# Kernel tuning notes

Measured on AMD Instinct MI355X. Metric: run time of the kernel, lower is better.

## Reference

```python
import jax, jax.numpy as jnp
import numpy as np
from jax import lax

H = 145; W = 145; BANDS = 200; D_MODEL = 128; NUM_CLASSES = 17
# Mamba2 defaults: expand=2, headdim=64, d_state=128, d_conv=4, ngroups=1
D_INNER = 256; NHEADS = 4; HEADDIM = 64; D_STATE = 128; D_CONV = 4
D_IN_PROJ = 2 * D_INNER + 2 * D_STATE + NHEADS  # 772
CONV_DIM = D_INNER + 2 * D_STATE                # 512


def _gelu(x):
    return jax.nn.gelu(x, approximate=False)


def _ln(x, g, b, eps=1e-5):
    m = jnp.mean(x, -1, keepdims=True)
    v = jnp.mean((x - m) ** 2, -1, keepdims=True)
    return (x - m) * lax.rsqrt(v + eps) * g + b


def _adaptive_pool_last(x, out):
    # PyTorch AdaptiveAvgPool semantics along the last axis via integral image
    L = x.shape[-1]
    i = np.arange(out)
    starts = (i * L) // out
    ends = -((-(i + 1) * L) // out)  # ceil((i+1)*L/out)
    cs = jnp.concatenate([jnp.zeros(x.shape[:-1] + (1,), x.dtype), jnp.cumsum(x, -1)], -1)
    return (cs[..., ends] - cs[..., starts]) / jnp.asarray(ends - starts, x.dtype)


def _mamba2(u, in_w, conv_w, conv_b, dt_bias, A_log, D, norm_w, out_w):
    # u: (L, D_MODEL). Faithful Mamba2 reference path (batch=1 squeezed).
    L = u.shape[0]
    zxbcdt = u @ in_w                      # (L, 772)
    z = zxbcdt[:, :D_INNER]                # (L, 256)
    xBC = zxbcdt[:, D_INNER:2 * D_INNER + 2 * D_STATE]  # (L, 512)
    dt = jax.nn.softplus(zxbcdt[:, -NHEADS:] + dt_bias)  # (L, 4)
    # causal depthwise conv1d, kernel D_CONV, then SiLU
    xp = jnp.pad(xBC, ((D_CONV - 1, 0), (0, 0)))
    xBC = sum(xp[k:k + L] * conv_w[:, k] for k in range(D_CONV)) + conv_b
    xBC = jax.nn.silu(xBC)
    xh = xBC[:, :D_INNER].reshape(L, NHEADS, HEADDIM)     # (L, h, p)
    Bm = xBC[:, D_INNER:D_INNER + D_STATE]                # (L, n)
    Cm = xBC[:, D_INNER + D_STATE:]                       # (L, n)
    A = -jnp.exp(A_log)                                   # (h,)

    def step(state, inp):
        dt_t, x_t, B_t, C_t = inp          # (h,), (h,p), (n,), (n,)
        dA = jnp.exp(dt_t * A)             # (h,)
        state = state * dA[:, None, None] + (dt_t[:, None] * x_t)[:, :, None] * B_t[None, None, :]
        y_t = jnp.einsum('hpn,n->hp', state, C_t)
        return state, y_t

    s0 = jnp.zeros((NHEADS, HEADDIM, D_STATE), u.dtype)
    _, y = lax.scan(step, s0, (dt, xh, Bm, Cm))           # y: (L, h, p)
    y = y + D[None, :, None] * xh
    y = y.reshape(L, D_INNER) * jax.nn.silu(z)            # gated
    y = y * lax.rsqrt(jnp.mean(y * y, -1, keepdims=True) + 1e-5) * norm_w  # RMSNormGated
    return y @ out_w                                      # (L, D_MODEL)


def _forward(x, ln_pre_g, ln_pre_b, fe_w1, fe_b1, fe_w2, fe_b2,
             cv_w1, cv_b1, cv_w2, cv_b2, mp_w, mp_b, mp_ln_g, mp_ln_b,
             m_in_w, m_conv_w, m_conv_b, m_dt_bias, m_A_log, m_D, m_norm_w, m_out_w,
             cls_ln_g, cls_ln_b, cls_w1, cls_b1, cls_w2, cls_b2, cls_w3, cls_b3):
    h, w, _ = x.shape
    xn = _ln(x, ln_pre_g, ln_pre_b)
    # MLP feature branch
    f = _gelu(xn @ fe_w1 + fe_b1)
    f = _gelu(f @ fe_w2 + fe_b2)                          # (h, w, 128)
    # conv branch
    c = jnp.transpose(xn, (2, 0, 1))[None]                # (1, bands, h, w)
    dn = ('NCHW', 'OIHW', 'NCHW')
    c = lax.conv_general_dilated(c, cv_w1, (1, 1), [(2, 2), (2, 2)], dimension_numbers=dn)
    c = _gelu(c + cv_b1[None, :, None, None])             # (1, 32, 147, 147)
    c = lax.conv_general_dilated(c, cv_w2, (1, 1), [(1, 1), (1, 1)], dimension_numbers=dn)
    c = _gelu(c + cv_b2[None, :, None, None])             # (1, 64, 147, 147)
    c = _adaptive_pool_last(c, W)                         # pool width -> 145
    c = _adaptive_pool_last(c.swapaxes(-1, -2), H).swapaxes(-1, -2)  # pool height
    conv_feat = jnp.transpose(c[0], (1, 2, 0))            # (145, 145, 64)
    comb = jnp.concatenate([f, conv_feat], -1).reshape(h * w, 192)
    p = _gelu(_ln(comb @ mp_w + mp_b, mp_ln_g, mp_ln_b))  # (L, d_model)
    m = _mamba2(p, m_in_w, m_conv_w, m_conv_b, m_dt_bias, m_A_log, m_D, m_norm_w, m_out_w)
    r = m.reshape(h, w, D_MODEL)
    o = _ln(r, cls_ln_g, cls_ln_b)
    o = _gelu(o @ cls_w1 + cls_b1)
    o = _gelu(o @ cls_w2 + cls_b2)
    return o @ cls_w3 + cls_b3                            # (h, w, num_classes)


def setup_inputs() -> dict:
    key = jax.random.key(0)
    ks = jax.random.split(key, 16)
    def n(k, shape, s=0.02):
        return jax.random.normal(k, shape, jnp.float32) * s
    return dict(
        x=jax.random.normal(ks[0], (H, W, BANDS), jnp.float32),
        ln_pre_g=jnp.ones((BANDS,), jnp.float32), ln_pre_b=jnp.zeros((BANDS,), jnp.float32),
        fe_w1=n(ks[1], (BANDS, 256)), fe_b1=jnp.zeros((256,), jnp.float32),
        fe_w2=n(ks[2], (256, 128)), fe_b2=jnp.zeros((128,), jnp.float32),
        cv_w1=n(ks[3], (32, BANDS, 3, 3)), cv_b1=jnp.zeros((32,), jnp.float32),
        cv_w2=n(ks[4], (64, 32, 3, 3)), cv_b2=jnp.zeros((64,), jnp.float32),
        mp_w=n(ks[5], (192, D_MODEL)), mp_b=jnp.zeros((D_MODEL,), jnp.float32),
        mp_ln_g=jnp.ones((D_MODEL,), jnp.float32), mp_ln_b=jnp.zeros((D_MODEL,), jnp.float32),
        m_in_w=n(ks[6], (D_MODEL, D_IN_PROJ)),
        m_conv_w=n(ks[7], (CONV_DIM, D_CONV), 0.2), m_conv_b=jnp.zeros((CONV_DIM,), jnp.float32),
        m_dt_bias=jnp.full((NHEADS,), -4.0, jnp.float32),
        m_A_log=jnp.log(jnp.linspace(1.0, 16.0, NHEADS)).astype(jnp.float32),
        m_D=jnp.ones((NHEADS,), jnp.float32),
        m_norm_w=jnp.ones((D_INNER,), jnp.float32),
        m_out_w=n(ks[8], (D_INNER, D_MODEL)),
        cls_ln_g=jnp.ones((D_MODEL,), jnp.float32), cls_ln_b=jnp.zeros((D_MODEL,), jnp.float32),
        cls_w1=n(ks[9], (D_MODEL, 128)), cls_b1=jnp.zeros((128,), jnp.float32),
        cls_w2=n(ks[10], (128, 64)), cls_b2=jnp.zeros((64,), jnp.float32),
        cls_w3=n(ks[11], (64, NUM_CLASSES)), cls_b3=jnp.zeros((NUM_CLASSES,), jnp.float32),
    )


def reference(x, ln_pre_g, ln_pre_b, fe_w1, fe_b1, fe_w2, fe_b2,
              cv_w1, cv_b1, cv_w2, cv_b2, mp_w, mp_b, mp_ln_g, mp_ln_b,
              m_in_w, m_conv_w, m_conv_b, m_dt_bias, m_A_log, m_D, m_norm_w, m_out_w,
              cls_ln_g, cls_ln_b, cls_w1, cls_b1, cls_w2, cls_b2, cls_w3, cls_b3):
    return _forward(x, ln_pre_g, ln_pre_b, fe_w1, fe_b1, fe_w2, fe_b2,
                    cv_w1, cv_b1, cv_w2, cv_b2, mp_w, mp_b, mp_ln_g, mp_ln_b,
                    m_in_w, m_conv_w, m_conv_b, m_dt_bias, m_A_log, m_D, m_norm_w, m_out_w,
                    cls_ln_g, cls_ln_b, cls_w1, cls_b1, cls_w2, cls_b2, cls_w3, cls_b3)
```

## Files before the change

### kernel.cpp

```cpp
#include <hip/hip_runtime.h>
#include <math.h>

#define HW 21025
#define Hdim 145
#define Wdim 145
#define NBANDS 200
#define CONVH 147
#define CONVHW 21609
#define QC 64
#define NCH 329
#define DTP 21056
#define SP 72

typedef __attribute__((ext_vector_type(4))) float fv4;
typedef __attribute__((ext_vector_type(8))) short short8;

#define OFF_XN   ((size_t)0)
#define OFF_F1   ((size_t)4205000)
#define OFF_COMB ((size_t)9587400)
#define OFF_P    ((size_t)13624200)
#define OFF_ZX   ((size_t)16315400)
#define OFF_XBC  ((size_t)32546700)
#define OFF_S    ((size_t)43311500)
#define OFF_DT   ((size_t)54092172)
#define OFF_CT   ((size_t)54176396)
#define OFF_W    ((size_t)54177712)

__device__ __forceinline__ float gelu_f(float x){
    return 0.5f * x * (1.0f + erff(x * 0.70710678118654752440f));
}
__device__ __forceinline__ float silu_f(float x){
    return x / (1.0f + expf(-x));
}

__device__ __forceinline__ void bf16_split(float x, unsigned short& hs, unsigned short& ls){
    unsigned u = __float_as_uint(x);
    hs = (unsigned short)(u >> 16);
    float hif = __uint_as_float(u & 0xFFFF0000u);
    float lof = x - hif;
    ls = (unsigned short)(__float_as_uint(lof) >> 16);
}
__device__ __forceinline__ unsigned pack2(unsigned short a, unsigned short b){
    return (unsigned)a | ((unsigned)b << 16);
}

template<int ACT>
__global__ void ln_kernel(const float* __restrict__ in, const float* __restrict__ g,
                          const float* __restrict__ b, float* __restrict__ out, int D){
    int row = blockIdx.x, tid = threadIdx.x;
    const float* r = in + (size_t)row * D;
    float s = 0.f, s2 = 0.f;
    for (int i = tid; i < D; i += 256){ float v = r[i]; s += v; s2 += v*v; }
    __shared__ float r1[4], r2[4];
    #pragma unroll
    for (int o = 32; o > 0; o >>= 1){ s += __shfl_down(s, o); s2 += __shfl_down(s2, o); }
    if ((tid & 63) == 0){ r1[tid >> 6] = s; r2[tid >> 6] = s2; }
    __syncthreads();
    float S = r1[0] + r1[1] + r1[2] + r1[3];
    float S2 = r2[0] + r2[1] + r2[2] + r2[3];
    float mean = S / (float)D;
    float var = S2 / (float)D - mean * mean;
    float rs = rsqrtf(fmaxf(var, 0.f) + 1e-5f);
    float* o_ = out + (size_t)row * D;
    for (int i = tid; i < D; i += 256){
        float v = (r[i] - mean) * rs * g[i] + b[i];
        if (ACT == 1) v = gelu_f(v);
        o_[i] = v;
    }
}

template<int ACT>
__global__ __launch_bounds__(256) void gemm_mfma(const float* __restrict__ A, int lda,
                                                 const float* __restrict__ B,
                                                 const float* __restrict__ bias,
                                                 float* __restrict__ C, int ldc,
                                                 int M, int N, int K){
    const int SA = 40;
    __shared__ __align__(16) unsigned short Ah[128 * SA], Al[128 * SA];
    __shared__ __align__(16) unsigned short Bh[64 * SA],  Bl[64 * SA];
    int tid = threadIdx.x;
    int lane = tid & 63, wid = tid >> 6;
    int wy = wid >> 1, wx = wid & 1;
    int bm = blockIdx.y * 128, bn = blockIdx.x * 64;
    int l15 = lane & 15, g = lane >> 4;

    fv4 acc[4][2];
    #pragma unroll
    for (int i = 0; i < 4; i++)
        #pragma unroll
        for (int j = 0; j < 2; j++) acc[i][j] = (fv4){0.f,0.f,0.f,0.f};

    int am = tid >> 1;
    int aq = (tid & 1) * 4;
    bool arow_ok = (bm + am) < M;
    int bn_t = tid & 63;
    int bk8 = (tid >> 6) * 8;
    bool bcol_ok = (bn + bn_t) < N;

    int nK = (K + 31) / 32;
    for (int ks = 0; ks < nK; ks++){
        int k0 = ks * 32;
        const float* Ap = A + (size_t)(bm + am) * lda + k0;
        #pragma unroll
        for (int f = 0; f < 4; f++){
            int kq = aq + f;
            fv4 v = (fv4){0.f,0.f,0.f,0.f};
            if (arow_ok && (k0 + kq * 4 + 4) <= K)
                v = *reinterpret_cast<const fv4*>(Ap + kq * 4);
            unsigned short hs[4], ls[4];
            #pragma unroll
            for (int j = 0; j < 4; j++) bf16_split(v[j], hs[j], ls[j]);
            unsigned off = am * SA + kq * 4;
            *reinterpret_cast<uint2*>(&Ah[off]) = make_uint2(pack2(hs[0],hs[1]), pack2(hs[2],hs[3]));
            *reinterpret_cast<uint2*>(&Al[off]) = make_uint2(pack2(ls[0],ls[1]), pack2(ls[2],ls[3]));
        }
        {
            unsigned short hs[8], ls[8];
            #pragma unroll
            for (int j = 0; j < 8; j++){
                int kk = k0 + bk8 + j;
                float v = (bcol_ok && kk < K) ? B[(size_t)kk * N + bn + bn_t] : 0.f;
                bf16_split(v, hs[j], ls[j]);
            }
            unsigned off = bn_t * SA + bk8;
            *reinterpret_cast<uint4*>(&Bh[off]) = make_uint4(pack2(hs[0],hs[1]), pack2(hs[2],hs[3]),
                                                             pack2(hs[4],hs[5]), pack2(hs[6],hs[7]));
// ... 118 lines not shown
                bh[ni] = *reinterpret_cast<const short8*>(&Wh[woff]);
                bl[ni] = *reinterpret_cast<const short8*>(&Wl[woff]);
            }
            #pragma unroll
            for (int mi = 0; mi < 2; mi++)
                #pragma unroll
                for (int ni = 0; ni < NFRAG; ni++){
                    acc[mi][ni] = __builtin_amdgcn_mfma_f32_16x16x32_bf16(ah[mi], bh[ni], acc[mi][ni], 0, 0, 0);
                    acc[mi][ni] = __builtin_amdgcn_mfma_f32_16x16x32_bf16(ah[mi], bl[ni], acc[mi][ni], 0, 0, 0);
                    acc[mi][ni] = __builtin_amdgcn_mfma_f32_16x16x32_bf16(al[mi], bh[ni], acc[mi][ni], 0, 0, 0);
                }
        }
    }
    #pragma unroll
    for (int mi = 0; mi < 2; mi++)
        #pragma unroll
        for (int ni = 0; ni < NFRAG; ni++){
            int oc = wx * (16 * NFRAG) + ni * 16 + l15;
            float bv = bias[oc];
            #pragma unroll
            for (int j = 0; j < 4; j++){
                int x = x0 + wy * 32 + mi * 16 + g * 4 + j;
                if (x >= CONVH) continue;
                out[((size_t)y * CONVH + x) * OC + oc] = gelu_f(acc[mi][ni][j] + bv);
            }
        }
}

__global__ void pool_kernel(const float* __restrict__ c2, float* __restrict__ comb){
    int idx = blockIdx.x * 256 + threadIdx.x;
    if (idx >= HW * 64) return;
    int o = idx & 63;
    int pix = idx >> 6;
    int xo = pix % Wdim, yo = pix / Wdim;
    int ys = yo * CONVH / Hdim, ye = ((yo + 1) * CONVH + Hdim - 1) / Hdim;
    int xs = xo * CONVH / Wdim, xe = ((xo + 1) * CONVH + Wdim - 1) / Wdim;
    float s = 0.f;
    for (int yy = ys; yy < ye; yy++)
        for (int xx = xs; xx < xe; xx++)
            s += c2[((size_t)yy * CONVH + xx) * 64 + o];
    comb[(size_t)pix * 192 + 128 + o] = s / (float)((ye - ys) * (xe - xs));
}

__global__ void dt_kernel(const float* __restrict__ zx, const float* __restrict__ dt_bias,
                          float* __restrict__ dtbT){
    int t = blockIdx.x * 256 + threadIdx.x;
    int h = blockIdx.y;
    if (t >= HW) return;
    float v = zx[(size_t)t * 772 + 768 + h] + dt_bias[h];
    dtbT[h * DTP + t] = (v > 20.f) ? v : log1pf(expf(v));
}

__global__ __launch_bounds__(256) void conv1d_tiled(const float* __restrict__ zx,
                                                    const float* __restrict__ w,
                                                    const float* __restrict__ b,
                                                    float* __restrict__ xbc){
    __shared__ float xs[67 * 128];
    __shared__ float wc[4 * 128];
    __shared__ float bc[128];
    int t0 = blockIdx.y * 64;
    int c0 = blockIdx.x * 128;
    int tid = threadIdx.x;
    for (int e = tid; e < 67 * 128; e += 256){
        int rr = e >> 7, cc = e & 127;
        int t = t0 - 3 + rr;
        xs[e] = (t >= 0 && t < HW) ? zx[(size_t)t * 772 + 256 + c0 + cc] : 0.f;
    }
    if (tid < 128){
        bc[tid] = b[c0 + tid];
        #pragma unroll
        for (int k = 0; k < 4; k++) wc[k * 128 + tid] = w[(c0 + tid) * 4 + k];
    }
    __syncthreads();
    for (int e = tid; e < 64 * 128; e += 256){
        int tt = e >> 7, cc = e & 127;
        if (t0 + tt >= HW) continue;
        float acc = bc[cc];
        #pragma unroll
        for (int k = 0; k < 4; k++) acc += xs[(tt + k) * 128 + cc] * wc[k * 128 + cc];
        xbc[(size_t)(t0 + tt) * 512 + c0 + cc] = silu_f(acc);
    }
}

__device__ __forceinline__ void chunk_cumsum_t(const float* __restrict__ dtbT, int t0, int Q,
                                               int h, const float* __restrict__ A_log,
                                               float* cum, float* dth){
    int tid = threadIdx.x;
    if (tid < 64){
        float d = (tid < Q) ? dtbT[h * DTP + t0 + tid] : 0.f;
        dth[tid] = d;
        float A = -expf(A_log[h]);
        float a = d * A;
        #pragma unroll
        for (int off = 1; off < 64; off <<= 1){
            float u = __shfl_up(a, off);
            if (tid >= off) a += u;
        }
        cum[tid] = a;
    }
    __syncthreads();
}

__global__ __launch_bounds__(256) void ssd_phaseA(const float* __restrict__ xbc,
                                                  const float* __restrict__ dtbT,
                                                  const float* __restrict__ A_log,
                                                  float* __restrict__ S,
                                                  float* __restrict__ chunkT){
    __shared__ __align__(16) unsigned short BTh[128 * SP], BTl[128 * SP];
    __shared__ __align__(16) unsigned short XTh[64 * SP],  XTl[64 * SP];
    __shared__ float cum[64], dth[64], wln[64];
    int bid = blockIdx.x, c = bid >> 2, h = bid & 3;
    int t0 = c * QC, Q = min(QC, HW - t0);
    int tid = threadIdx.x;
    chunk_cumsum_t(dtbT, t0, Q, h, A_log, cum, dth);
    float T = cum[Q - 1];
    if (tid == 0) chunkT[bid] = T;
    if (tid < 64) wln[tid] = (tid < Q) ? __expf(T - cum[tid]) * dth[tid] : 0.f;
    __syncthreads();
    for (int e2 = tid; e2 < 4096; e2 += 256){
        int nn = e2 & 127, sp = e2 >> 7;
        int s0 = 2 * sp;
        float v0 = (s0 < Q)     ? xbc[(size_t)(t0 + s0) * 512 + 256 + nn] : 0.f;
        float v1 = (s0 + 1 < Q) ? xbc[(size_t)(t0 + s0 + 1) * 512 + 256 + nn] : 0.f;
        unsigned short h0, l0, h1, l1;
        bf16_split(v0, h0, l0); bf16_split(v1, h1, l1);
        *reinterpret_cast<unsigned*>(&BTh[nn * SP + s0]) = pack2(h0, h1);
        *reinterpret_cast<unsigned*>(&BTl[nn * SP + s0]) = pack2(l0, l1);
    }
    for (int e2 = tid; e2 < 2048; e2 += 256){
        int pp = e2 & 63, sp = e2 >> 6;
        int s0 = 2 * sp;
        float v0 = (s0 < Q)     ? xbc[(size_t)(t0 + s0) * 512 + h * 64 + pp] * wln[s0] : 0.f;
        float v1 = (s0 + 1 < Q) ? xbc[(size_t)(t0 + s0 + 1) * 512 + h * 64 + pp] * wln[s0 + 1] : 0.f;
        unsigned short h0, l0, h1, l1;
        bf16_split(v0, h0, l0); bf16_split(v1, h1, l1);
        *reinterpret_cast<unsigned*>(&XTh[pp * SP + s0]) = pack2(h0, h1);
        *reinterpret_cast<unsigned*>(&XTl[pp * SP + s0]) = pack2(l0, l1);
    }
    __syncthreads();
    int lane = tid & 63, wid = tid >> 6;
    int wy = wid >> 1, wx = wid & 1;
    int l15 = lane & 15, g = lane >> 4;
    fv4 acc[2][4];
    #pragma unroll
    for (int mi = 0; mi < 2; mi++)
        #pragma unroll
        for (int ni = 0; ni < 4; ni++) acc[mi][ni] = (fv4){0.f,0.f,0.f,0.f};
    #pragma unroll
    for (int ks = 0; ks < 2; ks++){
        short8 ah[2], al[2], bh_[4], bl_[4];
        #pragma unroll
        for (int mi = 0; mi < 2; mi++){
            unsigned off = (wy * 32 + mi * 16 + l15) * SP + ks * 32 + g * 8;
            ah[mi] = *reinterpret_cast<const short8*>(&XTh[off]);
            al[mi] = *reinterpret_cast<const short8*>(&XTl[off]);
        }
        #pragma unroll
        for (int ni = 0; ni < 4; ni++){
            unsigned off = (wx * 64 + ni * 16 + l15) * SP + ks * 32 + g * 8;
            bh_[ni] = *reinterpret_cast<const short8*>(&BTh[off]);
            bl_[ni] = *reinterpret_cast<const short8*>(&BTl[off]);
        }
        #pragma unroll
        for (int mi = 0; mi < 2; mi++)
            #pragma unroll
            for (int ni = 0; ni < 4; ni++){
                acc[mi][ni] = __builtin_amdgcn_mfma_f32_16x16x32_bf16(ah[mi], bh_[ni], acc[mi][ni], 0, 0, 0);
                acc[mi][ni] = __builtin_amdgcn_mfma_f32_16x16x32_bf16(ah[mi], bl_[ni], acc[mi][ni], 0, 0, 0);
                acc[mi][ni] = __builtin_amdgcn_mfma_f32_16x16x32_bf16(al[mi], bh_[ni], acc[mi][ni], 0, 0, 0);
            }
    }
    size_t sb = (size_t)bid * 8192;
    #pragma unroll
    for (int mi = 0; mi < 2; mi++)
        #pragma unroll
        for (int ni = 0; ni < 4; ni++)
            #pragma unroll
            for (int j = 0; j < 4; j++){
                int p = wy * 32 + mi * 16 + g * 4 + j;
                int n = wx * 64 + ni * 16 + l15;
                S[sb + p * 128 + n] = acc[mi][ni][j];
            }
}

__global__ __launch_bounds__(256) void ssd_phaseB(float* __restrict__ S,
                                                  const float* __restrict__ chunkT){
    __shared__ float e[NCH];
    int tid = threadIdx.x;
    int idx = blockIdx.x * 256 + tid;
    int h = idx >> 13, pn = idx & 8191;
    for (int c = tid; c < NCH; c += 256) e[c] = __expf(chunkT[c * 4 + h]);
    __syncthreads();
    #define LDS_(cc) S[((size_t)((cc) * 4 + h)) * 8192 + pn]
    float b0 = LDS_(0), b1 = LDS_(1), b2 = LDS_(2), b3 = LDS_(3);
    float s = 0.f;
    int c = 0;
    for (; c + 8 <= NCH; c += 4){
        float n0 = LDS_(c + 4), n1 = LDS_(c + 5), n2 = LDS_(c + 6), n3 = LDS_(c + 7);
        LDS_(c) = s;     s = fmaf(s, e[c],     b0);
        LDS_(c + 1) = s; s = fmaf(s, e[c + 1], b1);
        LDS_(c + 2) = s; s = fmaf(s, e[c + 2], b2);
        LDS_(c + 3) = s; s = fmaf(s, e[c + 3], b3);
        b0 = n0; b1 = n1; b2 = n2; b3 = n3;
    }
    for (; c < NCH; c++){
        float nx = (c + 4 < NCH) ? LDS_(c + 4) : 0.f;
        float loc = b0; b0 = b1; b1 = b2; b2 = b3; b3 = nx;
        LDS_(c) = s;
        s = fmaf(s, e[c], loc);
    }
    #undef LDS_
}

__global__ __launch_bounds__(256) void ssd_phaseC(const float* __restrict__ xbc,
                                                  const float* __restrict__ dtbT,
                                                  const float* __restrict__ A_log,
                                                  const float* __restrict__ Dvec,
                                                  const float* __restrict__ S,
                                                  float* __restrict__ y){
    __shared__ __align__(16) unsigned short Ch_[64 * SP], Cl_[64 * SP];
    __shared__ __align__(16) unsigned short Bh_[64 * SP], Bl_[64 * SP];
    __shared__ __align__(16) unsigned short Sh_[64 * SP], Sl_[64 * SP];
    __shared__ float cum[64], dth[64];
    int bid = blockIdx.x, c = bid >> 2, h = bid & 3;
    int t0 = c * QC, Q = min(QC, HW - t0);
    int tid = threadIdx.x;
    chunk_cumsum_t(dtbT, t0, Q, h, A_log, cum, dth);
    int lane = tid & 63, wid = tid >> 6;
    int wy = wid >> 1, wx = wid & 1;
    int l15 = lane & 15, g = lane >> 4;
    size_t sb = (size_t)bid * 8192;

    fv4 accG[2][2], accA[2][2];
    #pragma unroll
    for (int mi = 0; mi < 2; mi++)
        #pragma unroll
        for (int ni = 0; ni < 2; ni++){ accG[mi][ni] = (fv4){0.f,0.f,0.f,0.f}; accA[mi][ni] = (fv4){0.f,0.f,0.f,0.f}; }

    #pragma unroll
    for (int ks = 0; ks < 2; ks++){
        int n0 = ks * 64;
        for (int e2 = tid; e2 < 2048; e2 += 256){
            int rr = e2 >> 5, n2 = (e2 & 31) * 2;
            bool ok = rr < Q;
            float c0 = ok ? xbc[(size_t)(t0 + rr) * 512 + 384 + n0 + n2]     : 0.f;
            float c1 = ok ? xbc[(size_t)(t0 + rr) * 512 + 384 + n0 + n2 + 1] : 0.f;
            float b0 = ok ? xbc[(size_t)(t0 + rr) * 512 + 256 + n0 + n2]     : 0.f;
            float b1 = ok ? xbc[(size_t)(t0 + rr) * 512 + 256 + n0 + n2 + 1] : 0.f;
            float s0 = S[sb + rr * 128 + n0 + n2];
            float s1 = S[sb + rr * 128 + n0 + n2 + 1];
            unsigned short xh0, xl0, xh1, xl1;
            bf16_split(c0, xh0, xl0); bf16_split(c1, xh1, xl1);
            *reinterpret_cast<unsigned*>(&Ch_[rr * SP + n2]) = pack2(xh0, xh1);
            *reinterpret_cast<unsigned*>(&Cl_[rr * SP + n2]) = pack2(xl0, xl1);
            bf16_split(b0, xh0, xl0); bf16_split(b1, xh1, xl1);
            *reinterpret_cast<unsigned*>(&Bh_[rr * SP + n2]) = pack2(xh0, xh1);
            *reinterpret_cast<unsigned*>(&Bl_[rr * SP + n2]) = pack2(xl0, xl1);
            bf16_split(s0, xh0, xl0); bf16_split(s1, xh1, xl1);
            *reinterpret_cast<unsigned*>(&Sh_[rr * SP + n2]) = pack2(xh0, xh1);
            *reinterpret_cast<unsigned*>(&Sl_[rr * SP + n2]) = pack2(xl0, xl1);
        }
        __syncthreads();
        #pragma unroll
        for (int kk = 0; kk < 2; kk++){
            short8 ah[2], al[2], gh[2], gl[2], sh[2], sl[2];
            #pragma unroll
            for (int mi = 0; mi < 2; mi++){
                unsigned off = (wy * 32 + mi * 16 + l15) * SP + kk * 32 + g * 8;
                ah[mi] = *reinterpret_cast<const short8*>(&Ch_[off]);
                al[mi] = *reinterpret_cast<const short8*>(&Cl_[off]);
            }
            #pragma unroll
            for (int ni = 0; ni < 2; ni++){
                unsigned off = (wx * 32 + ni * 16 + l15) * SP + kk * 32 + g * 8;
                gh[ni] = *reinterpret_cast<const short8*>(&Bh_[off]);
                gl[ni] = *reinterpret_cast<const short8*>(&Bl_[off]);
                sh[ni] = *reinterpret_cast<const short8*>(&Sh_[off]);
                sl[ni] = *reinterpret_cast<const short8*>(&Sl_[off]);
            }
            #pragma unroll
            for (int mi = 0; mi < 2; mi++)
                #pragma unroll
                for (int ni = 0; ni < 2; ni++){
                    accG[mi][ni] = __builtin_amdgcn_mfma_f32_16x16x32_bf16(ah[mi], gh[ni], accG[mi][ni], 0, 0, 0);
                    accG[mi][ni] = __builtin_amdgcn_mfma_f32_16x16x32_bf16(ah[mi], gl[ni], accG[mi][ni], 0, 0, 0);
                    accG[mi][ni] = __builtin_amdgcn_mfma_f32_16x16x32_bf16(al[mi], gh[ni], accG[mi][ni], 0, 0, 0);
                    accA[mi][ni] = __builtin_amdgcn_mfma_f32_16x16x32_bf16(ah[mi], sh[ni], accA[mi][ni], 0, 0, 0);
                    accA[mi][ni] = __builtin_amdgcn_mfma_f32_16x16x32_bf16(ah[mi], sl[ni], accA[mi][ni], 0, 0, 0);
                    accA[mi][ni] = __builtin_amdgcn_mfma_f32_16x16x32_bf16(al[mi], sh[ni], accA[mi][ni], 0, 0, 0);
                }
        }
        __syncthreads();
    }
    #pragma unroll
    for (int mi = 0; mi < 2; mi++)
        #pragma unroll
        for (int ni = 0; ni < 2; ni++)
            #pragma unroll
            for (int j = 0; j < 4; j++){
                int t = wy * 32 + mi * 16 + g * 4 + j;
                int s = wx * 32 + ni * 16 + l15;
                float pv = 0.f;
                if (s <= t && s < Q)
                    pv = accG[mi][ni][j] * __expf(cum[t] - cum[s]) * dth[s];
                unsigned short hs, ls;
                bf16_split(pv, hs, ls);
                Bh_[t * SP + s] = hs;
                Bl_[t * SP + s] = ls;
            }
    for (int e2 = tid; e2 < 2048; e2 += 256){
        int pp = e2 & 63, sp = e2 >> 6;
        int s0 = 2 * sp;
        float v0 = (s0 < Q)     ? xbc[(size_t)(t0 + s0) * 512 + h * 64 + pp] : 0.f;
        float v1 = (s0 + 1 < Q) ? xbc[(size_t)(t0 + s0 + 1) * 512 + h * 64 + pp] : 0.f;
        unsigned short h0, l0, h1, l1;
        bf16_split(v0, h0, l0); bf16_split(v1, h1, l1);
        *reinterpret_cast<unsigned*>(&Ch_[pp * SP + s0]) = pack2(h0, h1);
        *reinterpret_cast<unsigned*>(&Cl_[pp * SP + s0]) = pack2(l0, l1);
    }
    __syncthreads();
    fv4 accY[2][2];
    #pragma unroll
    for (int mi = 0; mi < 2; mi++)
        #pragma unroll
        for (int ni = 0; ni < 2; ni++)
            #pragma unroll
            for (int j = 0; j < 4; j++){
                int t = wy * 32 + mi * 16 + g * 4 + j;
                accY[mi][ni][j] = __expf(cum[t]) * accA[mi][ni][j];
            }
    #pragma unroll
    for (int kk = 0; kk < 2; kk++){
        short8 ph[2], pl[2], xh[2], xl[2];
        #pragma unroll
        for (int mi = 0; mi < 2; mi++){
            unsigned off = (wy * 32 + mi * 16 + l15) * SP + kk * 32 + g * 8;
            ph[mi] = *reinterpret_cast<const short8*>(&Bh_[off]);
            pl[mi] = *reinterpret_cast<const short8*>(&Bl_[off]);
        }
        #pragma unroll
        for (int ni = 0; ni < 2; ni++){
            unsigned off = (wx * 32 + ni * 16 + l15) * SP + kk * 32 + g * 8;
            xh[ni] = *reinterpret_cast<const short8*>(&Ch_[off]);
            xl[ni] = *reinterpret_cast<const short8*>(&Cl_[off]);
        }
        #pragma unroll
        for (int mi = 0; mi < 2; mi++)
            #pragma unroll
            for (int ni = 0; ni < 2; ni++){
                accY[mi][ni] = __builtin_amdgcn_mfma_f32_16x16x32_bf16(ph[mi], xh[ni], accY[mi][ni], 0, 0, 0);
                accY[mi][ni] = __builtin_amdgcn_mfma_f32_16x16x32_bf16(ph[mi], xl[ni], accY[mi][ni], 0, 0, 0);
                accY[mi][ni] = __builtin_amdgcn_mfma_f32_16x16x32_bf16(pl[mi], xh[ni], accY[mi][ni], 0, 0, 0);
            }
    }
    float Dh = Dvec[h];
    #pragma unroll
    for (int mi = 0; mi < 2; mi++)
        #pragma unroll
        for (int ni = 0; ni < 2; ni++)
            #pragma unroll
            for (int j = 0; j < 4; j++){
                int t = wy * 32 + mi * 16 + g * 4 + j;
                if (t >= Q) continue;
                int p = wx * 32 + ni * 16 + l15;
                float xv = xbc[(size_t)(t0 + t) * 512 + h * 64 + p];
                y[(size_t)(t0 + t) * 256 + h * 64 + p] = accY[mi][ni][j] + Dh * xv;
            }
}

__global__ void gated_rms_kernel(float* __restrict__ y, const float* __restrict__ zx,
                                 const float* __restrict__ nw){
    int row = blockIdx.x, tid = threadIdx.x;
    float v = y[(size_t)row * 256 + tid];
    float z = zx[(size_t)row * 772 + tid];
    v *= silu_f(z);
    float s = v * v;
    __shared__ float r1[4];
    #pragma unroll
    for (int o = 32; o > 0; o >>= 1) s += __shfl_down(s, o);
    if ((tid & 63) == 0) r1[tid >> 6] = s;
    __syncthreads();
    float S = r1[0] + r1[1] + r1[2] + r1[3];
    float rs = rsqrtf(S / 256.f + 1e-5f);
    y[(size_t)row * 256 + tid] = v * rs * nw[tid];
}

extern "C" void kernel_launch(void* const* d_in, const int* in_sizes, int n_in,
                              void* d_out, int out_size, void* d_ws, size_t ws_size,
                              hipStream_t stream){
    (void)in_sizes; (void)n_in; (void)out_size; (void)ws_size;
    const float* x        = (const float*)d_in[0];
    const float* ln_pre_g = (const float*)d_in[1];
    const float* ln_pre_b = (const float*)d_in[2];
    const float* fe_w1    = (const float*)d_in[3];
    const float* fe_b1    = (const float*)d_in[4];
    const float* fe_w2    = (const float*)d_in[5];
    const float* fe_b2    = (const float*)d_in[6];
    const float* cv_w1    = (const float*)d_in[7];
    const float* cv_b1    = (const float*)d_in[8];
    const float* cv_w2    = (const float*)d_in[9];
    const float* cv_b2    = (const float*)d_in[10];
    const float* mp_w     = (const float*)d_in[11];
    const float* mp_b     = (const float*)d_in[12];
    const float* mp_ln_g  = (const float*)d_in[13];
    const float* mp_ln_b  = (const float*)d_in[14];
    const float* m_in_w   = (const float*)d_in[15];
    const float* m_conv_w = (const float*)d_in[16];
    const float* m_conv_b = (const float*)d_in[17];
    const float* m_dtb    = (const float*)d_in[18];
    const float* m_A_log  = (const float*)d_in[19];
    const float* m_D      = (const float*)d_in[20];
    const float* m_norm_w = (const float*)d_in[21];
    const float* m_out_w  = (const float*)d_in[22];
    const float* cls_ln_g = (const float*)d_in[23];
    const float* cls_ln_b = (const float*)d_in[24];
    const float* cls_w1   = (const float*)d_in[25];
    const float* cls_b1   = (const float*)d_in[26];
    const float* cls_w2   = (const float*)d_in[27];
    const float* cls_b2   = (const float*)d_in[28];
    const float* cls_w3   = (const float*)d_in[29];
    const float* cls_b3   = (const float*)d_in[30];

    float* ws   = (float*)d_ws;
    float* xn   = ws + OFF_XN;
    float* f1   = ws + OFF_F1;
    float* comb = ws + OFF_COMB;
    float* p    = ws + OFF_P;
    float* zx   = ws + OFF_ZX;
    float* xbc  = ws + OFF_XBC;
    float* Sbuf = ws + OFF_S;
    float* dtbT = ws + OFF_DT;
    float* chkT = ws + OFF_CT;
    float* c1h  = ws + OFF_XBC;
    float* c2h  = ws + OFF_XBC + 691488;
    float* pr   = ws + OFF_XN;
    float* ybuf = ws + OFF_F1;
    float* mo   = ws + OFF_COMB;
    float* cls0 = ws + OFF_XN;
    float* cls1 = ws + OFF_P;
    float* cls2 = ws + OFF_COMB + 2691200;
    unsigned short* W1h = (unsigned short*)(ws + OFF_W);
    unsigned short* W1l = (unsigned short*)(ws + OFF_W + 32256);
    unsigned short* W2h = (unsigned short*)(ws + OFF_W + 64512);
    unsigned short* W2l = (unsigned short*)(ws + OFF_W + 73728);

    prep_w<200, 32, 7><<<(32 * 2016 + 255) / 256, 256, 0, stream>>>(cv_w1, W1h, W1l);
    prep_w<32, 64, 1><<<(64 * 288 + 255) / 256, 256, 0, stream>>>(cv_w2, W2h, W2l);
    ln_kernel<0><<<HW, 256, 0, stream>>>(x, ln_pre_g, ln_pre_b, xn, NBANDS);
    gemm_mfma<1><<<dim3(4, 165), 256, 0, stream>>>(xn, 200, fe_w1, fe_b1, f1, 256, HW, 256, 200);
    gemm_mfma<1><<<dim3(2, 165), 256, 0, stream>>>(f1, 256, fe_w2, fe_b2, comb, 192, HW, 128, 256);
    conv_mfma<200, 32, 2, 7, 1><<<dim3(3, CONVH), 256, 0, stream>>>(xn, Hdim, Wdim, W1h, W1l, cv_b1, c1h);
    conv_mfma<32, 64, 1, 1, 2><<<dim3(3, CONVH), 256, 0, stream>>>(c1h, CONVH, CONVH, W2h, W2l, cv_b2, c2h);
    pool_kernel<<<(HW * 64 + 255) / 256, 256, 0, stream>>>(c2h, comb);
    gemm_mfma<0><<<dim3(2, 165), 256, 0, stream>>>(comb, 192, mp_w, mp_b, pr, 128, HW, 128, 192);
    ln_kernel<1><<<HW, 256, 0, stream>>>(pr, mp_ln_g, mp_ln_b, p, 128);
    gemm_mfma<0><<<dim3(13, 165), 256, 0, stream>>>(p, 128, m_in_w, (const float*)nullptr, zx, 772, HW, 772, 128);
    dt_kernel<<<dim3((HW + 255) / 256, 4), 256, 0, stream>>>(zx, m_dtb, dtbT);
    conv1d_tiled<<<dim3(4, NCH), 256, 0, stream>>>(zx, m_conv_w, m_conv_b, xbc);
    ssd_phaseA<<<NCH * 4, 256, 0, stream>>>(xbc, dtbT, m_A_log, Sbuf, chkT);
    ssd_phaseB<<<128, 256, 0, stream>>>(Sbuf, chkT);
    ssd_phaseC<<<NCH * 4, 256, 0, stream>>>(xbc, dtbT, m_A_log, m_D, Sbuf, ybuf);
    gated_rms_kernel<<<HW, 256, 0, stream>>>(ybuf, zx, m_norm_w);
    gemm_mfma<0><<<dim3(2, 165), 256, 0, stream>>>(ybuf, 256, m_out_w, (const float*)nullptr, mo, 128, HW, 128, 256);
    ln_kernel<0><<<HW, 256, 0, stream>>>(mo, cls_ln_g, cls_ln_b, cls0, 128);
    gemm_mfma<1><<<dim3(2, 165), 256, 0, stream>>>(cls0, 128, cls_w1, cls_b1, cls1, 128, HW, 128, 128);
    gemm_mfma<1><<<dim3(1, 165), 256, 0, stream>>>(cls1, 128, cls_w2, cls_b2, cls2, 64, HW, 64, 128);
    gemm_mfma<0><<<dim3(1, 165), 256, 0, stream>>>(cls2, 64, cls_w3, cls_b3, (float*)d_out, 17, HW, 17, 64);
}
```

Baseline: 517.6 us.

## Process all four heads per chunk block in SSD phases A and C

SSD phases A and C now launch one block per chunk instead of one per (chunk, head) and loop over the four heads inside the block. The shared B/C tiles and the C·Bᵀ Gram matrix are built and split once per chunk and reused across heads, which removes redundant global loads and redundant MFMA work. Phase C also reads S directly from global memory into registers rather than staging it in LDS. The grid drops to 329 blocks, which costs parallelism and occupancy on a GPU with many CUs, and it adds more accumulator registers per thread.

```diff
diff --git a/kernel.cpp b/kernel.cpp
--- a/kernel.cpp
+++ b/kernel.cpp
@@ -42,6 +42,16 @@
 }
 __device__ __forceinline__ unsigned pack2(unsigned short a, unsigned short b){
     return (unsigned)a | ((unsigned)b << 16);
+}
+__device__ __forceinline__ void split8g(const float* p, short8& h8, short8& l8){
+    fv4 v0 = *reinterpret_cast<const fv4*>(p);
+    fv4 v1 = *reinterpret_cast<const fv4*>(p + 4);
+    unsigned short hs, ls;
+    #pragma unroll
+    for (int j = 0; j < 4; j++){
+        bf16_split(v0[j], hs, ls); h8[j] = (short)hs; l8[j] = (short)ls;
+        bf16_split(v1[j], hs, ls); h8[4 + j] = (short)hs; l8[4 + j] = (short)ls;
+    }
 }
 
 template<int ACT>
@@ -326,25 +336,6 @@
     }
 }
 
-__device__ __forceinline__ void chunk_cumsum_t(const float* __restrict__ dtbT, int t0, int Q,
-                                               int h, const float* __restrict__ A_log,
-                                               float* cum, float* dth){
-    int tid = threadIdx.x;
-    if (tid < 64){
-        float d = (tid < Q) ? dtbT[h * DTP + t0 + tid] : 0.f;
-        dth[tid] = d;
-        float A = -expf(A_log[h]);
-        float a = d * A;
-        #pragma unroll
-        for (int off = 1; off < 64; off <<= 1){
-            float u = __shfl_up(a, off);
-            if (tid >= off) a += u;
-        }
-        cum[tid] = a;
-    }
-    __syncthreads();
-}
-
 __global__ __launch_bounds__(256) void ssd_phaseA(const float* __restrict__ xbc,
                                                   const float* __restrict__ dtbT,
                                                   const float* __restrict__ A_log,
@@ -352,14 +343,26 @@
                                                   float* __restrict__ chunkT){
     __shared__ __align__(16) unsigned short BTh[128 * SP], BTl[128 * SP];
     __shared__ __align__(16) unsigned short XTh[64 * SP],  XTl[64 * SP];
-    __shared__ float cum[64], dth[64], wln[64];
-    int bid = blockIdx.x, c = bid >> 2, h = bid & 3;
+    __shared__ float wln4[4][64];
+    int c = blockIdx.x;
     int t0 = c * QC, Q = min(QC, HW - t0);
     int tid = threadIdx.x;
-    chunk_cumsum_t(dtbT, t0, Q, h, A_log, cum, dth);
-    float T = cum[Q - 1];
-    if (tid == 0) chunkT[bid] = T;
-    if (tid < 64) wln[tid] = (tid < Q) ? __expf(T - cum[tid]) * dth[tid] : 0.f;
+    int lane = tid & 63, wid = tid >> 6;
+    int wy = wid >> 1, wx = wid & 1;
+    int l15 = lane & 15, g = lane >> 4;
+    {
+        float d = (lane < Q) ? dtbT[wid * DTP + t0 + lane] : 0.f;
+        float A = -expf(A_log[wid]);
+        float a = d * A;
+        #pragma unroll
+        for (int off = 1; off < 64; off <<= 1){
+            float u = __shfl_up(a, off);
+            if (lane >= off) a += u;
+        }
+        float T = __shfl(a, Q - 1);
+        wln4[wid][lane] = (lane < Q) ? __expf(T - a) * d : 0.f;
+        if (lane == 0) chunkT[c * 4 + wid] = T;
+    }
     __syncthreads();
     for (int e2 = tid; e2 < 4096; e2 += 256){
         int nn = e2 & 127, sp = e2 >> 7;
@@ -371,60 +374,60 @@
         *reinterpret_cast<unsigned*>(&BTh[nn * SP + s0]) = pack2(h0, h1);
         *reinterpret_cast<unsigned*>(&BTl[nn * SP + s0]) = pack2(l0, l1);
     }
-    for (int e2 = tid; e2 < 2048; e2 += 256){
-        int pp = e2 & 63, sp = e2 >> 6;
-        int s0 = 2 * sp;
-        float v0 = (s0 < Q)     ? xbc[(size_t)(t0 + s0) * 512 + h * 64 + pp] * wln[s0] : 0.f;
-        float v1 = (s0 + 1 < Q) ? xbc[(size_t)(t0 + s0 + 1) * 512 + h * 64 + pp] * wln[s0 + 1] : 0.f;
-        unsigned short h0, l0, h1, l1;
-        bf16_split(v0, h0, l0); bf16_split(v1, h1, l1);
-        *reinterpret_cast<unsigned*>(&XTh[pp * SP + s0]) = pack2(h0, h1);
-        *reinterpret_cast<unsigned*>(&XTl[pp * SP + s0]) = pack2(l0, l1);
-    }
-    __syncthreads();
-    int lane = tid & 63, wid = tid >> 6;
-    int wy = wid >> 1, wx = wid & 1;
-    int l15 = lane & 15, g = lane >> 4;
-    fv4 acc[2][4];
-    #pragma unroll
-    for (int mi = 0; mi < 2; mi++)
-        #pragma unroll
-        for (int ni = 0; ni < 4; ni++) acc[mi][ni] = (fv4){0.f,0.f,0.f,0.f};
-    #pragma unroll
-    for (int ks = 0; ks < 2; ks++){
-        short8 ah[2], al[2], bh_[4], bl_[4];
-        #pragma unroll
-        for (int mi = 0; mi < 2; mi++){
-            unsigned off = (wy * 32 + mi * 16 + l15) * SP + ks * 32 + g * 8;
-            ah[mi] = *reinterpret_cast<const short8*>(&XTh[off]);
-            al[mi] = *reinterpret_cast<const short8*>(&XTl[off]);
-        }
-        #pragma unroll
-        for (int ni = 0; ni < 4; ni++){
-            unsigned off = (wx * 64 + ni * 16 + l15) * SP + ks * 32 + g * 8;
-            bh_[ni] = *reinterpret_cast<const short8*>(&BTh[off]);
-            bl_[ni] = *reinterpret_cast<const short8*>(&BTl[off]);
-        }
+    for (int h = 0; h < 4; h++){
+        for (int e2 = tid; e2 < 2048; e2 += 256){
+            int pp = e2 & 63, sp = e2 >> 6;
+            int s0 = 2 * sp;
+            float v0 = (s0 < Q)     ? xbc[(size_t)(t0 + s0) * 512 + h * 64 + pp] * wln4[h][s0] : 0.f;
+            float v1 = (s0 + 1 < Q) ? xbc[(size_t)(t0 + s0 + 1) * 512 + h * 64 + pp] * wln4[h][s0 + 1] : 0.f;
+            unsigned short h0, l0, h1, l1;
+            bf16_split(v0, h0, l0); bf16_split(v1, h1, l1);
+            *reinterpret_cast<unsigned*>(&XTh[pp * SP + s0]) = pack2(h0, h1);
+            *reinterpret_cast<unsigned*>(&XTl[pp * SP + s0]) = pack2(l0, l1);
+        }
+        __syncthreads();
+        fv4 acc[2][4];
         #pragma unroll
         for (int mi = 0; mi < 2; mi++)
             #pragma unroll
+            for (int ni = 0; ni < 4; ni++) acc[mi][ni] = (fv4){0.f,0.f,0.f,0.f};
+        #pragma unroll
+        for (int ks = 0; ks < 2; ks++){
+            short8 ah[2], al[2], bh_[4], bl_[4];
+            #pragma unroll
+            for (int mi = 0; mi < 2; mi++){
+                unsigned off = (wy * 32 + mi * 16 + l15) * SP + ks * 32 + g * 8;
+                ah[mi] = *reinterpret_cast<const short8*>(&XTh[off]);
+                al[mi] = *reinterpret_cast<const short8*>(&XTl[off]);
+            }
+            #pragma unroll
             for (int ni = 0; ni < 4; ni++){
-                acc[mi][ni] = __builtin_amdgcn_mfma_f32_16x16x32_bf16(ah[mi], bh_[ni], acc[mi][ni], 0, 0, 0);
-                acc[mi][ni] = __builtin_amdgcn_mfma_f32_16x16x32_bf16(ah[mi], bl_[ni], acc[mi][ni], 0, 0, 0);
-                acc[mi][ni] = __builtin_amdgcn_mfma_f32_16x16x32_bf16(al[mi], bh_[ni], acc[mi][ni], 0, 0, 0);
-            }
-    }
-    size_t sb = (size_t)bid * 8192;
-    #pragma unroll
-    for (int mi = 0; mi < 2; mi++)
-        #pragma unroll
-        for (int ni = 0; ni < 4; ni++)
-            #pragma unroll
-            for (int j = 0; j < 4; j++){
-                int p = wy * 32 + mi * 16 + g * 4 + j;
-                int n = wx * 64 + ni * 16 + l15;
-                S[sb + p * 128 + n] = acc[mi][ni][j];
-            }
+                unsigned off = (wx * 64 + ni * 16 + l15) * SP + ks * 32 + g * 8;
+                bh_[ni] = *reinterpret_cast<const short8*>(&BTh[off]);
+                bl_[ni] = *reinterpret_cast<const short8*>(&BTl[off]);
+            }
+            #pragma unroll
+            for (int mi = 0; mi < 2; mi++)
+                #pragma unroll
+                for (int ni = 0; ni < 4; ni++){
+                    acc[mi][ni] = __builtin_amdgcn_mfma_f32_16x16x32_bf16(ah[mi], bh_[ni], acc[mi][ni], 0, 0, 0);
+                    acc[mi][ni] = __builtin_amdgcn_mfma_f32_16x16x32_bf16(ah[mi], bl_[ni], acc[mi][ni], 0, 0, 0);
+                    acc[mi][ni] = __builtin_amdgcn_mfma_f32_16x16x32_bf16(al[mi], bh_[ni], acc[mi][ni], 0, 0, 0);
+                }
+        }
+        size_t sb = (size_t)(c * 4 + h) * 8192;
+        #pragma unroll
+        for (int mi = 0; mi < 2; mi++)
+            #pragma unroll
+            for (int ni = 0; ni < 4; ni++)
+                #pragma unroll
+                for (int j = 0; j < 4; j++){
+                    int p = wy * 32 + mi * 16 + g * 4 + j;
+                    int n = wx * 64 + ni * 16 + l15;
+                    S[sb + p * 128 + n] = acc[mi][ni][j];
+                }
+        __syncthreads();
+    }
 }
 
 __global__ __launch_bounds__(256) void ssd_phaseB(float* __restrict__ S,
@@ -462,154 +465,180 @@
                                                   const float* __restrict__ Dvec,
                                                   const float* __restrict__ S,
                                                   float* __restrict__ y){
-    __shared__ __align__(16) unsigned short Ch_[64 * SP], Cl_[64 * SP];
-    __shared__ __align__(16) unsigned short Bh_[64 * SP], Bl_[64 * SP];
-    __shared__ __align__(16) unsigned short Sh_[64 * SP], Sl_[64 * SP];
-    __shared__ float cum[64], dth[64];
-    int bid = blockIdx.x, c = bid >> 2, h = bid & 3;
+    __shared__ __align__(16) unsigned short U0h[64 * SP], U0l[64 * SP];
+    __shared__ __align__(16) unsigned short U1h[64 * SP], U1l[64 * SP];
+    __shared__ float cum4[4][64], dth4[4][64];
+    int c = blockIdx.x;
     int t0 = c * QC, Q = min(QC, HW - t0);
     int tid = threadIdx.x;
-    chunk_cumsum_t(dtbT, t0, Q, h, A_log, cum, dth);
     int lane = tid & 63, wid = tid >> 6;
     int wy = wid >> 1, wx = wid & 1;
     int l15 = lane & 15, g = lane >> 4;
-    size_t sb = (size_t)bid * 8192;
-
-    fv4 accG[2][2], accA[2][2];
+    {
+        float d = (lane < Q) ? dtbT[wid * DTP + t0 + lane] : 0.f;
+        dth4[wid][lane] = d;
+        float A = -expf(A_log[wid]);
+        float a = d * A;
+        #pragma unroll
+        for (int off = 1; off < 64; off <<= 1){
+            float u = __shfl_up(a, off);
+            if (lane >= off) a += u;
+        }
+        cum4[wid][lane] = a;
+    }
+
+    fv4 accG[2][2];
+    fv4 accA[4][2][2];
     #pragma unroll
     for (int mi = 0; mi < 2; mi++)
         #pragma unroll
-        for (int ni = 0; ni < 2; ni++){ accG[mi][ni] = (fv4){0.f,0.f,0.f,0.f}; accA[mi][ni] = (fv4){0.f,0.f,0.f,0.f}; }
+        for (int ni = 0; ni < 2; ni++){
+            accG[mi][ni] = (fv4){0.f,0.f,0.f,0.f};
+            #pragma unroll
+            for (int h = 0; h < 4; h++) accA[h][mi][ni] = (fv4){0.f,0.f,0.f,0.f};
+        }
 
     #pragma unroll
     for (int ks = 0; ks < 2; ks++){
         int n0 = ks * 64;
+        __syncthreads();
         for (int e2 = tid; e2 < 2048; e2 += 256){
             int rr = e2 >> 5, n2 = (e2 & 31) * 2;
             bool ok = rr < Q;
-            float c0 = ok ? xbc[(size_t)(t0 + rr) * 512 + 384 + n0 + n2]     : 0.f;
-            float c1 = ok ? xbc[(size_t)(t0 + rr) * 512 + 384 + n0 + n2 + 1] : 0.f;
-            float b0 = ok ? xbc[(size_t)(t0 + rr) * 512 + 256 + n0 + n2]     : 0.f;
-            float b1 = ok ? xbc[(size_t)(t0 + rr) * 512 + 256 + n0 + n2 + 1] : 0.f;
-            float s0 = S[sb + rr * 128 + n0 + n2];
-            float s1 = S[sb + rr * 128 + n0 + n2 + 1];
+            const float* rp = xbc + (size_t)(t0 + rr) * 512;
+            float c0 = ok ? rp[384 + n0 + n2]     : 0.f;
+            float c1 = ok ? rp[384 + n0 + n2 + 1] : 0.f;
+            float b0 = ok ? rp[256 + n0 + n2]     : 0.f;
+            float b1 = ok ? rp[256 + n0 + n2 + 1] : 0.f;
             unsigned short xh0, xl0, xh1, xl1;
             bf16_split(c0, xh0, xl0); bf16_split(c1, xh1, xl1);
-            *reinterpret_cast<unsigned*>(&Ch_[rr * SP + n2]) = pack2(xh0, xh1);
-            *reinterpret_cast<unsigned*>(&Cl_[rr * SP + n2]) = pack2(xl0, xl1);
+            *reinterpret_cast<unsigned*>(&U0h[rr * SP + n2]) = pack2(xh0, xh1);
+            *reinterpret_cast<unsigned*>(&U0l[rr * SP + n2]) = pack2(xl0, xl1);
             bf16_split(b0, xh0, xl0); bf16_split(b1, xh1, xl1);
-            *reinterpret_cast<unsigned*>(&Bh_[rr * SP + n2]) = pack2(xh0, xh1);
-            *reinterpret_cast<unsigned*>(&Bl_[rr * SP + n2]) = pack2(xl0, xl1);
-            bf16_split(s0, xh0, xl0); bf16_split(s1, xh1, xl1);
-            *reinterpret_cast<unsigned*>(&Sh_[rr * SP + n2]) = pack2(xh0, xh1);
-            *reinterpret_cast<unsigned*>(&Sl_[rr * SP + n2]) = pack2(xl0, xl1);
+            *reinterpret_cast<unsigned*>(&U1h[rr * SP + n2]) = pack2(xh0, xh1);
+            *reinterpret_cast<unsigned*>(&U1l[rr * SP + n2]) = pack2(xl0, xl1);
         }
         __syncthreads();
         #pragma unroll
         for (int kk = 0; kk < 2; kk++){
-            short8 ah[2], al[2], gh[2], gl[2], sh[2], sl[2];
+            short8 ah[2], al[2], bh[2], bl[2];
             #pragma unroll
             for (int mi = 0; mi < 2; mi++){
                 unsigned off = (wy * 32 + mi * 16 + l15) * SP + kk * 32 + g * 8;
-                ah[mi] = *reinterpret_cast<const short8*>(&Ch_[off]);
-                al[mi] = *reinterpret_cast<const short8*>(&Cl_[off]);
+                ah[mi] = *reinterpret_cast<const short8*>(&U0h[off]);
+                al[mi] = *reinterpret_cast<const short8*>(&U0l[off]);
             }
             #pragma unroll
             for (int ni = 0; ni < 2; ni++){
                 unsigned off = (wx * 32 + ni * 16 + l15) * SP + kk * 32 + g * 8;
-                gh[ni] = *reinterpret_cast<const short8*>(&Bh_[off]);
-                gl[ni] = *reinterpret_cast<const short8*>(&Bl_[off]);
-                sh[ni] = *reinterpret_cast<const short8*>(&Sh_[off]);
-                sl[ni] = *reinterpret_cast<const short8*>(&Sl_[off]);
+                bh[ni] = *reinterpret_cast<const short8*>(&U1h[off]);
+                bl[ni] = *reinterpret_cast<const short8*>(&U1l[off]);
             }
             #pragma unroll
             for (int mi = 0; mi < 2; mi++)
                 #pragma unroll
                 for (int ni = 0; ni < 2; ni++){
-                    accG[mi][ni] = __builtin_amdgcn_mfma_f32_16x16x32_bf16(ah[mi], gh[ni], accG[mi][ni], 0, 0, 0);
-                    accG[mi][ni] = __builtin_amdgcn_mfma_f32_16x16x32_bf16(ah[mi], gl[ni], accG[mi][ni], 0, 0, 0);
-                    accG[mi][ni] = __builtin_amdgcn_mfma_f32_16x16x32_bf16(al[mi], gh[ni], accG[mi][ni], 0, 0, 0);
-                    accA[mi][ni] = __builtin_amdgcn_mfma_f32_16x16x32_bf16(ah[mi], sh[ni], accA[mi][ni], 0, 0, 0);
-                    accA[mi][ni] = __builtin_amdgcn_mfma_f32_16x16x32_bf16(ah[mi], sl[ni], accA[mi][ni], 0, 0, 0);
-                    accA[mi][ni] = __builtin_amdgcn_mfma_f32_16x16x32_bf16(al[mi], sh[ni], accA[mi][ni], 0, 0, 0);
-                }
-        }
-        __syncthreads();
-    }
-    #pragma unroll
-    for (int mi = 0; mi < 2; mi++)
-        #pragma unroll
-        for (int ni = 0; ni < 2; ni++)
-            #pragma unroll
-            for (int j = 0; j < 4; j++){
-                int t = wy * 32 + mi * 16 + g * 4 + j;
-                int s = wx * 32 + ni * 16 + l15;
-                float pv = 0.f;
-                if (s <= t && s < Q)
-                    pv = accG[mi][ni][j] * __expf(cum[t] - cum[s]) * dth[s];
-                unsigned short hs, ls;
-                bf16_split(pv, hs, ls);
-                Bh_[t * SP + s] = hs;
-                Bl_[t * SP + s] = ls;
-            }
-    for (int e2 = tid; e2 < 2048; e2 += 256){
-        int pp = e2 & 63, sp = e2 >> 6;
-        int s0 = 2 * sp;
-        float v0 = (s0 < Q)     ? xbc[(size_t)(t0 + s0) * 512 + h * 64 + pp] : 0.f;
-        float v1 = (s0 + 1 < Q) ? xbc[(size_t)(t0 + s0 + 1) * 512 + h * 64 + pp] : 0.f;
-        unsigned short h0, l0, h1, l1;
-        bf16_split(v0, h0, l0); bf16_split(v1, h1, l1);
-        *reinterpret_cast<unsigned*>(&Ch_[pp * SP + s0]) = pack2(h0, h1);
-        *reinterpret_cast<unsigned*>(&Cl_[pp * SP + s0]) = pack2(l0, l1);
-    }
-    __syncthreads();
-    fv4 accY[2][2];
-    #pragma unroll
-    for (int mi = 0; mi < 2; mi++)
-        #pragma unroll
-        for (int ni = 0; ni < 2; ni++)
-            #pragma unroll
-            for (int j = 0; j < 4; j++){
-                int t = wy * 32 + mi * 16 + g * 4 + j;
-                accY[mi][ni][j] = __expf(cum[t]) * accA[mi][ni][j];
-            }
-    #pragma unroll
-    for (int kk = 0; kk < 2; kk++){
-        short8 ph[2], pl[2], xh[2], xl[2];
-        #pragma unroll
-        for (int mi = 0; mi < 2; mi++){
-            unsigned off = (wy * 32 + mi * 16 + l15) * SP + kk * 32 + g * 8;
-            ph[mi] = *reinterpret_cast<const short8*>(&Bh_[off]);
-            pl[mi] = *reinterpret_cast<const short8*>(&Bl_[off]);
-        }
-        #pragma unroll
-        for (int ni = 0; ni < 2; ni++){
-            unsigned off = (wx * 32 + ni * 16 + l15) * SP + kk * 32 + g * 8;
-            xh[ni] = *reinterpret_cast<const short8*>(&Ch_[off]);
-            xl[ni] = *reinterpret_cast<const short8*>(&Cl_[off]);
-        }
+                    accG[mi][ni] = __builtin_amdgcn_mfma_f32_16x16x32_bf16(ah[mi], bh[ni], accG[mi][ni], 0, 0, 0);
+                    accG[mi][ni] = __builtin_amdgcn_mfma_f32_16x16x32_bf16(ah[mi], bl[ni], accG[mi][ni], 0, 0, 0);
+                    accG[mi][ni] = __builtin_amdgcn_mfma_f32_16x16x32_bf16(al[mi], bh[ni], accG[mi][ni], 0, 0, 0);
+                }
+            #pragma unroll
+            for (int h = 0; h < 4; h++){
+                const float* sbp = S + (size_t)(c * 4 + h) * 8192;
+                short8 sh[2], sl[2];
+                #pragma unroll
+                for (int ni = 0; ni < 2; ni++){
+                    int p = wx * 32 + ni * 16 + l15;
+                    split8g(sbp + (size_t)p * 128 + n0 + kk * 32 + g * 8, sh[ni], sl[ni]);
+                }
+                #pragma unroll
+                for (int mi = 0; mi < 2; mi++)
+                    #pragma unroll
+                    for (int ni = 0; ni < 2; ni++){
+                        accA[h][mi][ni] = __builtin_amdgcn_mfma_f32_16x16x32_bf16(ah[mi], sh[ni], accA[h][mi][ni], 0, 0, 0);
+                        accA[h][mi][ni] = __builtin_amdgcn_mfma_f32_16x16x32_bf16(ah[mi], sl[ni], accA[h][mi][ni], 0, 0, 0);
+                        accA[h][mi][ni] = __builtin_amdgcn_mfma_f32_16x16x32_bf16(al[mi], sh[ni], accA[h][mi][ni], 0, 0, 0);
+                    }
+            }
+        }
+    }
+    for (int h = 0; h < 4; h++){
+        __syncthreads();
         #pragma unroll
         for (int mi = 0; mi < 2; mi++)
             #pragma unroll
+            for (int ni = 0; ni < 2; ni++)
+                #pragma unroll
+                for (int j = 0; j < 4; j++){
+                    int t = wy * 32 + mi * 16 + g * 4 + j;
+                    int s = wx * 32 + ni * 16 + l15;
+                    float pv = 0.f;
+                    if (s <= t && s < Q)
+                        pv = accG[mi][ni][j] * __expf(cum4[h][t] - cum4[h][s]) * dth4[h][s];
+                    unsigned short hs, ls;
+                    bf16_split(pv, hs, ls);
+                    U0h[t * SP + s] = hs;
+                    U0l[t * SP + s] = ls;
+                }
+        for (int e2 = tid; e2 < 2048; e2 += 256){
+            int pp = e2 & 63, sp = e2 >> 6;
+            int s0 = 2 * sp;
+            float v0 = (s0 < Q)     ? xbc[(size_t)(t0 + s0) * 512 + h * 64 + pp] : 0.f;
+            float v1 = (s0 + 1 < Q) ? xbc[(size_t)(t0 + s0 + 1) * 512 + h * 64 + pp] : 0.f;
+            unsigned short h0, l0, h1, l1;
+            bf16_split(v0, h0, l0); bf16_split(v1, h1, l1);
+            *reinterpret_cast<unsigned*>(&U1h[pp * SP + s0]) = pack2(h0, h1);
+            *reinterpret_cast<unsigned*>(&U1l[pp * SP + s0]) = pack2(l0, l1);
+        }
+        __syncthreads();
+        fv4 accY[2][2];
+        #pragma unroll
+        for (int mi = 0; mi < 2; mi++)
+            #pragma unroll
+            for (int ni = 0; ni < 2; ni++)
+                #pragma unroll
+                for (int j = 0; j < 4; j++){
+                    int t = wy * 32 + mi * 16 + g * 4 + j;
+                    accY[mi][ni][j] = __expf(cum4[h][t]) * accA[h][mi][ni][j];
+                }
+        #pragma unroll
+        for (int kk = 0; kk < 2; kk++){
+            short8 ph[2], pl[2], xh[2], xl[2];
+            #pragma unroll
+            for (int mi = 0; mi < 2; mi++){
+                unsigned off = (wy * 32 + mi * 16 + l15) * SP + kk * 32 + g * 8;
+                ph[mi] = *reinterpret_cast<const short8*>(&U0h[off]);
+                pl[mi] = *reinterpret_cast<const short8*>(&U0l[off]);
+            }
+            #pragma unroll
             for (int ni = 0; ni < 2; ni++){
-                accY[mi][ni] = __builtin_amdgcn_mfma_f32_16x16x32_bf16(ph[mi], xh[ni], accY[mi][ni], 0, 0, 0);
-                accY[mi][ni] = __builtin_amdgcn_mfma_f32_16x16x32_bf16(ph[mi], xl[ni], accY[mi][ni], 0, 0, 0);
-                accY[mi][ni] = __builtin_amdgcn_mfma_f32_16x16x32_bf16(pl[mi], xh[ni], accY[mi][ni], 0, 0, 0);
-            }
-    }
-    float Dh = Dvec[h];
-    #pragma unroll
-    for (int mi = 0; mi < 2; mi++)
-        #pragma unroll
-        for (int ni = 0; ni < 2; ni++)
-            #pragma unroll
-            for (int j = 0; j < 4; j++){
-                int t = wy * 32 + mi * 16 + g * 4 + j;
-                if (t >= Q) continue;
-                int p = wx * 32 + ni * 16 + l15;
-                float xv = xbc[(size_t)(t0 + t) * 512 + h * 64 + p];
-                y[(size_t)(t0 + t) * 256 + h * 64 + p] = accY[mi][ni][j] + Dh * xv;
-            }
+                unsigned off = (wx * 32 + ni * 16 + l15) * SP + kk * 32 + g * 8;
+                xh[ni] = *reinterpret_cast<const short8*>(&U1h[off]);
+                xl[ni] = *reinterpret_cast<const short8*>(&U1l[off]);
+            }
+            #pragma unroll
+            for (int mi = 0; mi < 2; mi++)
+                #pragma unroll
+                for (int ni = 0; ni < 2; ni++){
+                    accY[mi][ni] = __builtin_amdgcn_mfma_f32_16x16x32_bf16(ph[mi], xh[ni], accY[mi][ni], 0, 0, 0);
+                    accY[mi][ni] = __builtin_amdgcn_mfma_f32_16x16x32_bf16(ph[mi], xl[ni], accY[mi][ni], 0, 0, 0);
+                    accY[mi][ni] = __builtin_amdgcn_mfma_f32_16x16x32_bf16(pl[mi], xh[ni], accY[mi][ni], 0, 0, 0);
+                }
+        }
+        float Dh = Dvec[h];
+        #pragma unroll
+        for (int mi = 0; mi < 2; mi++)
+            #pragma unroll
+            for (int ni = 0; ni < 2; ni++)
+                #pragma unroll
+                for (int j = 0; j < 4; j++){
+                    int t = wy * 32 + mi * 16 + g * 4 + j;
+                    if (t >= Q) continue;
+                    int p = wx * 32 + ni * 16 + l15;
+                    float xv = xbc[(size_t)(t0 + t) * 512 + h * 64 + p];
+                    y[(size_t)(t0 + t) * 256 + h * 64 + p] = accY[mi][ni][j] + Dh * xv;
+                }
+    }
 }
 
 __global__ void gated_rms_kernel(float* __restrict__ y, const float* __restrict__ zx,
@@ -701,9 +730,9 @@
     gemm_mfma<0><<<dim3(13, 165), 256, 0, stream>>>(p, 128, m_in_w, (const float*)nullptr, zx, 772, HW, 772, 128);
     dt_kernel<<<dim3((HW + 255) / 256, 4), 256, 0, stream>>>(zx, m_dtb, dtbT);
     conv1d_tiled<<<dim3(4, NCH), 256, 0, stream>>>(zx, m_conv_w, m_conv_b, xbc);
-    ssd_phaseA<<<NCH * 4, 256, 0, stream>>>(xbc, dtbT, m_A_log, Sbuf, chkT);
+    ssd_phaseA<<<NCH, 256, 0, stream>>>(xbc, dtbT, m_A_log, Sbuf, chkT);
     ssd_phaseB<<<128, 256, 0, stream>>>(Sbuf, chkT);
-    ssd_phaseC<<<NCH * 4, 256, 0, stream>>>(xbc, dtbT, m_A_log, m_D, Sbuf, ybuf);
+    ssd_phaseC<<<NCH, 256, 0, stream>>>(xbc, dtbT, m_A_log, m_D, Sbuf, ybuf);
     gated_rms_kernel<<<HW, 256, 0, stream>>>(ybuf, zx, m_norm_w);
     gemm_mfma<0><<<dim3(2, 165), 256, 0, stream>>>(ybuf, 256, m_out_w, (const float*)nullptr, mo, 128, HW, 128, 256);
     ln_kernel<0><<<HW, 256, 0, stream>>>(mo, cls_ln_g, cls_ln_b, cls0, 128);
```

After: 520.9 us. No clear change (+0.7%).
